# Kernel optimization log

Measured on AMD Instinct MI355X. Metric: run time of the kernel, lower is better.

The kernel has to match this reference:

```python
import jax, jax.numpy as jnp
import numpy as np

NUM_HEADS = 8
DIMS = 512
SR = 2
EPS = 1e-6


def setup_inputs() -> dict:
    key = jax.random.key(0)
    ks = jax.random.split(key, 12)
    B, H, W, C = 4, 64, 64, DIMS
    s = 0.02
    return {
        "x": jax.random.normal(ks[0], (B, H * W, C), dtype=jnp.float32),
        "Wq": jax.random.normal(ks[1], (C, DIMS), dtype=jnp.float32) * s,
        "bq": jnp.zeros((DIMS,), jnp.float32),
        "Wk": jax.random.normal(ks[2], (C, DIMS), dtype=jnp.float32) * s,
        "bk": jnp.zeros((DIMS,), jnp.float32),
        "Wv": jax.random.normal(ks[3], (C, DIMS), dtype=jnp.float32) * s,
        "bv": jnp.zeros((DIMS,), jnp.float32),
        "Wp": jax.random.normal(ks[4], (DIMS, DIMS), dtype=jnp.float32) * s,
        "bp": jnp.zeros((DIMS,), jnp.float32),
        "sr_w": jax.random.normal(ks[5], (SR, SR, C, DIMS), dtype=jnp.float32) * s,  # HWIO
        "sr_b": jnp.zeros((DIMS,), jnp.float32),
        "ln_g": jnp.ones((DIMS,), jnp.float32),
        "ln_b": jnp.zeros((DIMS,), jnp.float32),
        "H": 64,
        "W": 64,
    }


def reference(x, Wq, bq, Wk, bk, Wv, bv, Wp, bp, sr_w, sr_b, ln_g, ln_b, H, W):
    B, N, C = x.shape
    hd = DIMS // NUM_HEADS

    # spatial-reduction of K/V: strided conv (kernel=stride=SR, SAME) + LayerNorm
    kv = x.reshape(B, H, W, C)
    kv = jax.lax.conv_general_dilated(
        kv, sr_w, window_strides=(SR, SR), padding="SAME",
        dimension_numbers=("NHWC", "HWIO", "NHWC")) + sr_b
    kv = kv.reshape(B, -1, C)  # [B, Nk, C], Nk = (H//SR)*(W//SR)
    mu = jnp.mean(kv, axis=-1, keepdims=True)
    var = jnp.mean(jnp.square(kv - mu), axis=-1, keepdims=True)
    kv = (kv - mu) * jax.lax.rsqrt(var + EPS) * ln_g + ln_b
    Nk = kv.shape[1]

    # NOTE: original splits heads as reshape(B, N, head_dims, num_heads) and
    # indexes the LAST axis per head -> head h sees channels d*NUM_HEADS+h.
    q = (x @ Wq + bq).reshape(B, N, hd, NUM_HEADS)
    k = (kv @ Wk + bk).reshape(B, Nk, hd, NUM_HEADS)
    v = (kv @ Wv + bv).reshape(B, Nk, hd, NUM_HEADS)

    scores = jnp.einsum("bqdh,bkdh->bhqk", q, k) / jnp.sqrt(jnp.float32(hd))
    w = jax.nn.softmax(scores, axis=-1)
    # concat of heads along channels -> (B, N, NUM_HEADS, hd) layout
    out = jnp.einsum("bhqk,bkdh->bqhd", w, v).reshape(B, N, DIMS)
    return out @ Wp + bp
```

## Files before the change

### kernel.cpp

```cpp
#include <hip/hip_runtime.h>


typedef __attribute__((ext_vector_type(8))) _Float16 f16x8;
typedef __attribute__((ext_vector_type(4))) _Float16 f16x4;
typedef __attribute__((ext_vector_type(4))) float f32x4;

#define EXP2F(x) __builtin_amdgcn_exp2f(x)

__device__ __forceinline__ void gload_lds16(const _Float16* g, _Float16* l)
{
    __builtin_amdgcn_global_load_lds(
        (const __attribute__((address_space(1))) void*)g,
        (__attribute__((address_space(3))) void*)l, 16, 0, 0);
}

__global__ __launch_bounds__(256)
void cvt_x_k(const float* __restrict__ in, _Float16* __restrict__ out)
{
    const size_t i = ((size_t)blockIdx.x * 256 + threadIdx.x) * 8;
    const float4 a = *(const float4*)(in + i);
    const float4 b = *(const float4*)(in + i + 4);
    f16x8 o;
    o[0] = (_Float16)a.x; o[1] = (_Float16)a.y; o[2] = (_Float16)a.z; o[3] = (_Float16)a.w;
    o[4] = (_Float16)b.x; o[5] = (_Float16)b.y; o[6] = (_Float16)b.z; o[7] = (_Float16)b.w;
    *(f16x8*)(out + i) = o;
}

__global__ __launch_bounds__(256)
void trans4_k(const float* __restrict__ Wq, const float* __restrict__ Wk,
              const float* __restrict__ Wv, const float* __restrict__ Wp,
              _Float16* __restrict__ wqt, _Float16* __restrict__ wkvt,
              _Float16* __restrict__ wpt)
{
    const float* src; _Float16* dst; int perm;
    switch (blockIdx.z) {
        case 0:  src = Wq; dst = wqt;           perm = 1; break;
        case 1:  src = Wk; dst = wkvt;          perm = 1; break;
        case 2:  src = Wv; dst = wkvt + 262144; perm = 0; break;
        default: src = Wp; dst = wpt;           perm = 0; break;
    }
    __shared__ float T[32][33];
    const int n0 = blockIdx.x * 32, k0 = blockIdx.y * 32;
    const int t = threadIdx.x;
    {
        const int r = t >> 3, c = (t & 7) * 4;
        const float4 v = *(const float4*)(src + (size_t)(k0 + r) * 512 + n0 + c);
        T[r][c + 0] = v.x; T[r][c + 1] = v.y; T[r][c + 2] = v.z; T[r][c + 3] = v.w;
    }
    __syncthreads();
    {
        const int j = t >> 3, i0 = (t & 7) * 4;
        const int n = n0 + j;
        const int nper = perm ? ((n & 7) * 64 + (n >> 3)) : n;
        f16x4 o;
        o[0] = (_Float16)T[i0 + 0][j];
        o[1] = (_Float16)T[i0 + 1][j];
        o[2] = (_Float16)T[i0 + 2][j];
        o[3] = (_Float16)T[i0 + 3][j];
        *(f16x4*)(dst + (size_t)nper * 512 + k0 + i0) = o;
    }
}

__global__ __launch_bounds__(256)
void trans_srw_k(const float* __restrict__ in, _Float16* __restrict__ out)
{
    __shared__ float T[32][33];
    const int n0 = blockIdx.x * 32, k0 = blockIdx.y * 32;
    const int t = threadIdx.x;
    {
        const int r = t >> 3, c = (t & 7) * 4;
        const float4 v = *(const float4*)(in + (size_t)(k0 + r) * 512 + n0 + c);
        T[r][c + 0] = v.x; T[r][c + 1] = v.y; T[r][c + 2] = v.z; T[r][c + 3] = v.w;
    }
    __syncthreads();
    {
        const int j = t >> 3, i0 = (t & 7) * 4;
        f16x4 o;
        o[0] = (_Float16)T[i0 + 0][j];
        o[1] = (_Float16)T[i0 + 1][j];
        o[2] = (_Float16)T[i0 + 2][j];
        o[3] = (_Float16)T[i0 + 3][j];
        *(f16x4*)(out + (size_t)(n0 + j) * 2048 + k0 + i0) = o;
    }
}

template<int MODE, bool CONV, int BM>
__global__ __launch_bounds__(256)
void gemm_f16(const _Float16* __restrict__ A, const _Float16* __restrict__ Wt,
              const float* __restrict__ bias, const float* __restrict__ bias2,
              void* __restrict__ Cv, void* __restrict__ Cv2)
{
    constexpr int K = CONV ? 2048 : 512;
    constexpr int MT = BM / 32;
    constexpr int AI = BM / 64;
    __shared__ __align__(16) _Float16 As[BM * 32];
    __shared__ __align__(16) _Float16 Ws[128 * 32];
    const int tid = threadIdx.x;
    const int wave = tid >> 6, lane = tid & 63;
    const int quad = lane >> 4, l15 = lane & 15;
    const int wm = wave >> 1, wn = wave & 1;
    const int wrow = wm * (BM / 2);
    const int m0 = blockIdx.y * BM, n0 = blockIdx.x * 128;

    f32x4 acc[MT][4] = {};

    for (int k0 = 0; k0 < K; k0 += 32) {
        __syncthreads();
        #pragma unroll
        for (int t = 0; t < AI; ++t) {
            const int ii = wave * AI + t;
            const int e = ii * 64 + lane;
            const int row = e >> 2, c8 = (e & 3) * 8;
            const _Float16* gp;
            if (CONV) {
                const int grow = m0 + row;
                const int b = grow >> 10, rem = grow & 1023;
                const int oh = rem >> 5, ow = rem & 31;
                const int gk = k0 + c8;
                const int ky = (gk >> 10) & 1, kx = (gk >> 9) & 1, ci = gk & 511;
                gp = A + ((size_t)((b * 64 + 2 * oh + ky) * 64) + (2 * ow + kx)) * 512 + ci;
            } else {
                gp = A + (size_t)(m0 + row) * K + k0 + c8;
            }
            gload_lds16(gp, &As[ii * 512]);
        }
        #pragma unroll
        for (int t = 0; t < 2; ++t) {
            const int ii = wave * 2 + t;
            const int e = ii * 64 + lane;
            const int row = e >> 2, c8 = (e & 3) * 8;
            gload_lds16(Wt + (size_t)(n0 + row) * K + k0 + c8, &Ws[ii * 512]);
        }
        __syncthreads();

        f16x8 af[MT], bf[4];
        #pragma unroll
        for (int mt = 0; mt < MT; ++mt)
            af[mt] = *(const f16x8*)&As[(wrow + mt * 16 + l15) * 32 + quad * 8];
        #pragma unroll
        for (int nt = 0; nt < 4; ++nt)
            bf[nt] = *(const f16x8*)&Ws[(wn * 64 + nt * 16 + l15) * 32 + quad * 8];
        #pragma unroll
        for (int mt = 0; mt < MT; ++mt)
            #pragma unroll
            for (int nt = 0; nt < 4; ++nt)
                acc[mt][nt] = __builtin_amdgcn_mfma_f32_16x16x32_f16(
                    af[mt], bf[nt], acc[mt][nt], 0, 0, 0);
    }

    #pragma unroll
    for (int nt = 0; nt < 4; ++nt) {
        const int gcol = n0 + wn * 64 + nt * 16 + l15;
        float bv;
        if (MODE == 6) bv = bias[(gcol & 63) * 8 + (gcol >> 6)];
        else if (MODE == 5) bv = (gcol < 512) ? bias[(gcol & 63) * 8 + (gcol >> 6)]
                                              : bias2[gcol - 512];
        else bv = bias[gcol];
        #pragma unroll
        for (int mt = 0; mt < MT; ++mt) {
            const int row0 = m0 + wrow + mt * 16 + quad * 4;
            if (MODE == 0) {
                #pragma unroll
                for (int r = 0; r < 4; ++r)
                    ((float*)Cv)[(size_t)(row0 + r) * 512 + gcol] = acc[mt][nt][r] + bv;
            } else if (MODE == 4 || MODE == 6) {
                #pragma unroll
                for (int r = 0; r < 4; ++r)
                    ((_Float16*)Cv)[(size_t)(row0 + r) * 512 + gcol] =
                        (_Float16)(acc[mt][nt][r] + bv);
            } else {
                if (gcol < 512) {
                    #pragma unroll
                    for (int r = 0; r < 4; ++r)
                        ((_Float16*)Cv)[(size_t)(row0 + r) * 512 + gcol] =
                            (_Float16)(acc[mt][nt][r] + bv);
                } else {
                    const int c = gcol - 512;
                    const int h = c & 7, d = c >> 3;
                    const int b_ = row0 >> 10, jj = row0 & 1023;
                    f16x4 o;
                    #pragma unroll
                    for (int r = 0; r < 4; ++r) o[r] = (_Float16)(acc[mt][nt][r] + bv);
                    *(f16x4*)((_Float16*)Cv2 +
                              ((size_t)(b_ * 8 + h) * 64 + d) * 1024 + jj) = o;
                }
            }
        }
    }
}

__global__ __launch_bounds__(256)
void ln_k(_Float16* __restrict__ buf, const float* __restrict__ g,
          const float* __restrict__ b)
{
    const int row = blockIdx.x;
    _Float16* p = buf + (size_t)row * 512;
    const int tid = threadIdx.x;
    const float vx = (float)p[tid * 2], vy = (float)p[tid * 2 + 1];
    float s = vx + vy, q = vx * vx + vy * vy;
    #pragma unroll
    for (int off = 32; off > 0; off >>= 1) {
        s += __shfl_xor(s, off);
        q += __shfl_xor(q, off);
    }
    __shared__ float ss[4], sq[4], stat[2];
    const int wid = tid >> 6;
    if ((tid & 63) == 0) { ss[wid] = s; sq[wid] = q; }
    __syncthreads();
    if (tid == 0) {
        const float S = ss[0] + ss[1] + ss[2] + ss[3];
        const float Q = sq[0] + sq[1] + sq[2] + sq[3];
        const float mu = S * (1.f / 512.f);
        const float var = fmaxf(Q * (1.f / 512.f) - mu * mu, 0.f);
        stat[0] = mu;
        stat[1] = rsqrtf(var + 1e-6f);
    }
    __syncthreads();
    const float mu = stat[0], rs = stat[1];
    const float2 gg = *(const float2*)(g + tid * 2);
    const float2 bb = *(const float2*)(b + tid * 2);
    p[tid * 2]     = (_Float16)((vx - mu) * rs * gg.x + bb.x);
    p[tid * 2 + 1] = (_Float16)((vy - mu) * rs * gg.y + bb.y);
}

__global__ __launch_bounds__(512)
void attn_mfma_k(const _Float16* __restrict__ qb,
                 const _Float16* __restrict__ kbuf,
                 const _Float16* __restrict__ vbuf,
                 _Float16* __restrict__ out)
{
    const int bh = blockIdx.y;
    const int qt = blockIdx.x;
    const int b = bh >> 3, h = bh & 7;
    const int tid = threadIdx.x;
    const int wave = tid >> 6, lane = tid & 63;
    const int quad = lane >> 4, l15 = lane & 15;

    __shared__ __align__(16) _Float16 Ks[2][64 * 72];
    __shared__ __align__(16) _Float16 Vs[2][64 * 72];
    __shared__ __align__(16) _Float16 Ps[8][16 * 72];

    const int qrow = b * 4096 + qt * 128 + wave * 16 + l15;
    const _Float16* qp = qb + (size_t)qrow * 512 + h * 64 + quad * 8;
    f16x8 qf0 = *(const f16x8*)qp;
    f16x8 qf1 = *(const f16x8*)(qp + 32);
    {
        const _Float16 qs = (_Float16)0.18033688f;
        #pragma unroll
        for (int i = 0; i < 8; ++i) { qf0[i] *= qs; qf1[i] *= qs; }
    }

    const int kr = tid >> 3, kc = (tid & 7) * 8;
    const _Float16* kg = kbuf + (size_t)(b * 1024 + kr) * 512 + h * 64 + kc;
    const _Float16* vg = vbuf + (size_t)(bh * 64 + kr) * 1024 + kc;

    f16x8 krg = *(const f16x8*)kg;
    f16x8 vrg = *(const f16x8*)vg;
    *(f16x8*)&Ks[0][kr * 72 + kc] = krg;
    *(f16x8*)&Vs[0][kr * 72 + kc] = vrg;

    float l_run[4] = {0.f, 0.f, 0.f, 0.f};
    f32x4 acc_o[4] = {};
    const int psw = l15 >> 2;

    for (int kt = 0; kt < 16; ++kt) {
        const int cur = kt & 1;
        __syncthreads();
        if (kt < 15) {
            krg = *(const f16x8*)(kg + (size_t)(kt + 1) * 64 * 512);
            vrg = *(const f16x8*)(vg + (kt + 1) * 64);
        }

        f32x4 s[4];
        #pragma unroll
        for (int ct = 0; ct < 4; ++ct) {
            f32x4 a = {};
            const f16x8 kf0 = *(const f16x8*)&Ks[cur][(ct * 16 + l15) * 72 + quad * 8];
            const f16x8 kf1 = *(const f16x8*)&Ks[cur][(ct * 16 + l15) * 72 + 32 + quad * 8];
            a = __builtin_amdgcn_mfma_f32_16x16x32_f16(qf0, kf0, a, 0, 0, 0);
            a = __builtin_amdgcn_mfma_f32_16x16x32_f16(qf1, kf1, a, 0, 0, 0);
            s[ct] = a;
        }

        #pragma unroll
        for (int ct = 0; ct < 4; ++ct) {
            const int pc = (2 * ct + (l15 >> 3));
            #pragma unroll
            for (int r = 0; r < 4; ++r) {
                const float p = EXP2F(s[ct][r]);
                Ps[wave][(quad * 4 + r) * 72 + (pc ^ quad) * 8 + (l15 & 7)] = (_Float16)p;
                l_run[r] += p;
            }
        }

        const f16x8 pf0 = *(const f16x8*)&Ps[wave][l15 * 72 + (quad ^ psw) * 8];
        const f16x8 pf1 = *(const f16x8*)&Ps[wave][l15 * 72 + 32 + (quad ^ psw) * 8];
        #pragma unroll
        for (int ct = 0; ct < 4; ++ct) {
            const f16x8 vf0 = *(const f16x8*)&Vs[cur][(ct * 16 + l15) * 72 + quad * 8];
            const f16x8 vf1 = *(const f16x8*)&Vs[cur][(ct * 16 + l15) * 72 + 32 + quad * 8];
            acc_o[ct] = __builtin_amdgcn_mfma_f32_16x16x32_f16(pf0, vf0, acc_o[ct], 0, 0, 0);
            acc_o[ct] = __builtin_amdgcn_mfma_f32_16x16x32_f16(pf1, vf1, acc_o[ct], 0, 0, 0);
        }

        if (kt < 15) {
            *(f16x8*)&Ks[cur ^ 1][kr * 72 + kc] = krg;
            *(f16x8*)&Vs[cur ^ 1][kr * 72 + kc] = vrg;
        }
    }

    float inv[4];
    #pragma unroll
    for (int r = 0; r < 4; ++r) {
        float ts = l_run[r];
        ts += __shfl_xor(ts, 1);
        ts += __shfl_xor(ts, 2);
        ts += __shfl_xor(ts, 4);
        ts += __shfl_xor(ts, 8);
        inv[r] = 1.0f / ts;
    }
    #pragma unroll
    for (int ct = 0; ct < 4; ++ct)
        #pragma unroll
        for (int r = 0; r < 4; ++r) {
            const int row = qt * 128 + wave * 16 + quad * 4 + r;
            const int col = h * 64 + ct * 16 + l15;
            out[((size_t)b * 4096 + row) * 512 + col] = (_Float16)(acc_o[ct][r] * inv[r]);
        }
}

extern "C" void kernel_launch(void* const* d_in, const int* in_sizes, int n_in,
                              void* d_out, int out_size, void* d_ws, size_t ws_size,
                              hipStream_t stream)
{
    const float* x   = (const float*)d_in[0];
    const float* Wq  = (const float*)d_in[1];
    const float* bq  = (const float*)d_in[2];
    const float* Wk  = (const float*)d_in[3];
    const float* bk  = (const float*)d_in[4];
    const float* Wv  = (const float*)d_in[5];
    const float* bv  = (const float*)d_in[6];
    const float* Wp  = (const float*)d_in[7];
    const float* bp  = (const float*)d_in[8];
    const float* srw = (const float*)d_in[9];
    const float* srb = (const float*)d_in[10];
    const float* lng = (const float*)d_in[11];
    const float* lnb = (const float*)d_in[12];

    _Float16* ws   = (_Float16*)d_ws;
    _Float16* xh   = ws;
    _Float16* atth = xh + 8388608;
    _Float16* kvh  = atth + 8388608;
    _Float16* kh   = kvh + 2097152;
    _Float16* vh   = kh + 2097152;
    _Float16* wqt  = vh + 2097152;
    _Float16* wkvt = wqt + 262144;
    _Float16* wpt  = wkvt + 524288;
    _Float16* srwt = wpt + 262144;
    _Float16* qh   = (_Float16*)d_out;

    cvt_x_k   <<<4096, 256, 0, stream>>>(x, xh);
    trans4_k  <<<dim3(16, 16, 4), 256, 0, stream>>>(Wq, Wk, Wv, Wp, wqt, wkvt, wpt);
    trans_srw_k<<<dim3(16, 64), 256, 0, stream>>>(srw, srwt);
    gemm_f16<4, true, 64><<<dim3(4, 64), 256, 0, stream>>>(
        xh, srwt, srb, nullptr, kvh, nullptr);
    ln_k<<<4096, 256, 0, stream>>>(kvh, lng, lnb);
    gemm_f16<6, false, 128><<<dim3(4, 128), 256, 0, stream>>>(
        xh, wqt, bq, nullptr, qh, nullptr);
    gemm_f16<5, false, 128><<<dim3(8, 32), 256, 0, stream>>>(
        kvh, wkvt, bk, bv, kh, vh);
    attn_mfma_k<<<dim3(32, 32), 512, 0, stream>>>(qh, kh, vh, atth);
    gemm_f16<0, false, 128><<<dim3(4, 128), 256, 0, stream>>>(
        atth, wpt, bp, nullptr, d_out, nullptr);
}
```

Baseline: 261.4 us.

## Keep softmax probabilities in registers via transposed S and double query rows per wave

The attention kernel now computes S^T (K as the A operand) so each lane's MFMA output can feed the PV MFMA (16x16x16) directly as its A operand. This removes the per-wave LDS round trip for P. Each wave now handles 32 query rows instead of 16, so every K/V fragment read from LDS is reused across two query subtiles, and the grid is halved. Row sums are reduced with cross-quad shuffles and redistributed before normalization. The cost is more registers per thread, which may lower occupancy, and the PV stage switches to smaller-K MFMAs.

```diff
diff --git a/kernel.cpp b/kernel.cpp
--- a/kernel.cpp
+++ b/kernel.cpp
@@ -238,16 +238,22 @@
 
     __shared__ __align__(16) _Float16 Ks[2][64 * 72];
     __shared__ __align__(16) _Float16 Vs[2][64 * 72];
-    __shared__ __align__(16) _Float16 Ps[8][16 * 72];
-
-    const int qrow = b * 4096 + qt * 128 + wave * 16 + l15;
+
+    const int qrow = b * 4096 + qt * 256 + wave * 32 + l15;
     const _Float16* qp = qb + (size_t)qrow * 512 + h * 64 + quad * 8;
-    f16x8 qf0 = *(const f16x8*)qp;
-    f16x8 qf1 = *(const f16x8*)(qp + 32);
+    f16x8 qf[2][2];
+    qf[0][0] = *(const f16x8*)qp;
+    qf[0][1] = *(const f16x8*)(qp + 32);
+    qf[1][0] = *(const f16x8*)(qp + 16 * 512);
+    qf[1][1] = *(const f16x8*)(qp + 16 * 512 + 32);
     {
         const _Float16 qs = (_Float16)0.18033688f;
         #pragma unroll
-        for (int i = 0; i < 8; ++i) { qf0[i] *= qs; qf1[i] *= qs; }
+        for (int su = 0; su < 2; ++su)
+            #pragma unroll
+            for (int g = 0; g < 2; ++g)
+                #pragma unroll
+                for (int i = 0; i < 8; ++i) qf[su][g][i] *= qs;
     }
 
     const int kr = tid >> 3, kc = (tid & 7) * 8;
@@ -259,9 +265,8 @@
     *(f16x8*)&Ks[0][kr * 72 + kc] = krg;
     *(f16x8*)&Vs[0][kr * 72 + kc] = vrg;
 
-    float l_run[4] = {0.f, 0.f, 0.f, 0.f};
-    f32x4 acc_o[4] = {};
-    const int psw = l15 >> 2;
+    float l_run[2] = {0.f, 0.f};
+    f32x4 acc[2][4] = {};
 
     for (int kt = 0; kt < 16; ++kt) {
         const int cur = kt & 1;
@@ -271,36 +276,36 @@
             vrg = *(const f16x8*)(vg + (kt + 1) * 64);
         }
 
-        f32x4 s[4];
+        f16x4 pa[2][4];
         #pragma unroll
         for (int ct = 0; ct < 4; ++ct) {
-            f32x4 a = {};
             const f16x8 kf0 = *(const f16x8*)&Ks[cur][(ct * 16 + l15) * 72 + quad * 8];
             const f16x8 kf1 = *(const f16x8*)&Ks[cur][(ct * 16 + l15) * 72 + 32 + quad * 8];
-            a = __builtin_amdgcn_mfma_f32_16x16x32_f16(qf0, kf0, a, 0, 0, 0);
-            a = __builtin_amdgcn_mfma_f32_16x16x32_f16(qf1, kf1, a, 0, 0, 0);
-            s[ct] = a;
-        }
-
-        #pragma unroll
-        for (int ct = 0; ct < 4; ++ct) {
-            const int pc = (2 * ct + (l15 >> 3));
-            #pragma unroll
-            for (int r = 0; r < 4; ++r) {
-                const float p = EXP2F(s[ct][r]);
-                Ps[wave][(quad * 4 + r) * 72 + (pc ^ quad) * 8 + (l15 & 7)] = (_Float16)p;
-                l_run[r] += p;
-            }
-        }
-
-        const f16x8 pf0 = *(const f16x8*)&Ps[wave][l15 * 72 + (quad ^ psw) * 8];
-        const f16x8 pf1 = *(const f16x8*)&Ps[wave][l15 * 72 + 32 + (quad ^ psw) * 8];
-        #pragma unroll
-        for (int ct = 0; ct < 4; ++ct) {
-            const f16x8 vf0 = *(const f16x8*)&Vs[cur][(ct * 16 + l15) * 72 + quad * 8];
-            const f16x8 vf1 = *(const f16x8*)&Vs[cur][(ct * 16 + l15) * 72 + 32 + quad * 8];
-            acc_o[ct] = __builtin_amdgcn_mfma_f32_16x16x32_f16(pf0, vf0, acc_o[ct], 0, 0, 0);
-            acc_o[ct] = __builtin_amdgcn_mfma_f32_16x16x32_f16(pf1, vf1, acc_o[ct], 0, 0, 0);
+            #pragma unroll
+            for (int su = 0; su < 2; ++su) {
+                f32x4 s = {};
+                s = __builtin_amdgcn_mfma_f32_16x16x32_f16(kf0, qf[su][0], s, 0, 0, 0);
+                s = __builtin_amdgcn_mfma_f32_16x16x32_f16(kf1, qf[su][1], s, 0, 0, 0);
+                const float p0 = EXP2F(s[0]), p1 = EXP2F(s[1]);
+                const float p2 = EXP2F(s[2]), p3 = EXP2F(s[3]);
+                l_run[su] += (p0 + p1) + (p2 + p3);
+                f16x4 t;
+                t[0] = (_Float16)p0; t[1] = (_Float16)p1;
+                t[2] = (_Float16)p2; t[3] = (_Float16)p3;
+                pa[su][ct] = t;
+            }
+        }
+
+        #pragma unroll
+        for (int nt = 0; nt < 4; ++nt) {
+            #pragma unroll
+            for (int ct = 0; ct < 4; ++ct) {
+                const f16x4 vf = *(const f16x4*)&Vs[cur][(nt * 16 + l15) * 72 + ct * 16 + quad * 4];
+                acc[0][nt] = __builtin_amdgcn_mfma_f32_16x16x16f16(
+                    pa[0][ct], vf, acc[0][nt], 0, 0, 0);
+                acc[1][nt] = __builtin_amdgcn_mfma_f32_16x16x16f16(
+                    pa[1][ct], vf, acc[1][nt], 0, 0, 0);
+            }
         }
 
         if (kt < 15) {
@@ -309,24 +314,25 @@
         }
     }
 
-    float inv[4];
     #pragma unroll
-    for (int r = 0; r < 4; ++r) {
-        float ts = l_run[r];
-        ts += __shfl_xor(ts, 1);
-        ts += __shfl_xor(ts, 2);
-        ts += __shfl_xor(ts, 4);
-        ts += __shfl_xor(ts, 8);
-        inv[r] = 1.0f / ts;
-    }
-    #pragma unroll
-    for (int ct = 0; ct < 4; ++ct)
-        #pragma unroll
-        for (int r = 0; r < 4; ++r) {
-            const int row = qt * 128 + wave * 16 + quad * 4 + r;
-            const int col = h * 64 + ct * 16 + l15;
-            out[((size_t)b * 4096 + row) * 512 + col] = (_Float16)(acc_o[ct][r] * inv[r]);
-        }
+    for (int su = 0; su < 2; ++su) {
+        float ts = l_run[su];
+        ts += __shfl_xor(ts, 16);
+        ts += __shfl_xor(ts, 32);
+        float inv[4];
+        #pragma unroll
+        for (int r = 0; r < 4; ++r)
+            inv[r] = 1.0f / __shfl(ts, quad * 4 + r, 16);
+        #pragma unroll
+        for (int nt = 0; nt < 4; ++nt)
+            #pragma unroll
+            for (int r = 0; r < 4; ++r) {
+                const int row = qt * 256 + wave * 32 + su * 16 + quad * 4 + r;
+                const int col = h * 64 + nt * 16 + l15;
+                out[((size_t)b * 4096 + row) * 512 + col] =
+                    (_Float16)(acc[su][nt][r] * inv[r]);
+            }
+    }
 }
 
 extern "C" void kernel_launch(void* const* d_in, const int* in_sizes, int n_in,
@@ -369,7 +375,7 @@
         xh, wqt, bq, nullptr, qh, nullptr);
     gemm_f16<5, false, 128><<<dim3(8, 32), 256, 0, stream>>>(
         kvh, wkvt, bk, bv, kh, vh);
-    attn_mfma_k<<<dim3(32, 32), 512, 0, stream>>>(qh, kh, vh, atth);
+    attn_mfma_k<<<dim3(16, 32), 512, 0, stream>>>(qh, kh, vh, atth);
     gemm_f16<0, false, 128><<<dim3(4, 128), 256, 0, stream>>>(
         atth, wpt, bp, nullptr, d_out, nullptr);
 }
```

Measured after the change: 247.0 us. 5.5% less time.
